# Optimization experiments

Measured on AMD Instinct MI355X. Metric: run time of the kernel, lower is better.

## Reference

```python
import jax, jax.numpy as jnp
import numpy as np

N_NODES = 30000
IN_DIM = 8
HIDDEN = 64
HEADS1 = 8
OUT_DIM = 8
NEG_SLOPE = 0.2


def _glorot(key, shape):
    fan_in, fan_out = shape[0], shape[-1]
    lim = jnp.sqrt(6.0 / (fan_in + fan_out))
    return jax.random.uniform(key, shape, jnp.float32, -lim, lim)


def setup_inputs() -> dict:
    key = jax.random.key(0)
    ks = jax.random.split(key, 12)
    x = jax.random.normal(ks[0], (N_NODES, IN_DIM), jnp.float32)
    edge_index = jax.random.randint(ks[1], (2, 300000), 0, N_NODES, jnp.int32)
    # layer 1: in=8, out=HIDDEN per head, 8 heads, concat
    W1l = _glorot(ks[2], (IN_DIM, HEADS1 * HIDDEN))
    W1r = _glorot(ks[3], (IN_DIM, HEADS1 * HIDDEN))
    a1 = _glorot(ks[4], (HEADS1, HIDDEN))
    b1 = jnp.zeros((HEADS1 * HIDDEN,), jnp.float32)
    # layer 2: in=HEADS1*HIDDEN, out=OUT_DIM, 1 head
    W2l = _glorot(ks[5], (HEADS1 * HIDDEN, OUT_DIM))
    W2r = _glorot(ks[6], (HEADS1 * HIDDEN, OUT_DIM))
    a2 = _glorot(ks[7], (1, OUT_DIM))
    b2 = jnp.zeros((OUT_DIM,), jnp.float32)
    return {"x": x, "edge_index": edge_index, "W1l": W1l, "W1r": W1r,
            "a1": a1, "b1": b1, "W2l": W2l, "W2r": W2r, "a2": a2, "b2": b2}


def gatv2_layer(x, src, dst, Wl, Wr, att, bias, heads, out_ch):
    n = x.shape[0]
    xl = (x @ Wl).reshape(n, heads, out_ch)   # messages (source side)
    xr = (x @ Wr).reshape(n, heads, out_ch)   # target side
    h = jax.nn.leaky_relu(xl[src] + xr[dst], NEG_SLOPE)   # [E,H,C]
    e = jnp.einsum('ehc,hc->eh', h, att)                  # [E,H]
    # segment softmax over incoming edges per destination node
    m = jax.ops.segment_max(e, dst, num_segments=n)
    p = jnp.exp(e - m[dst])
    denom = jax.ops.segment_sum(p, dst, num_segments=n)
    alpha = p / denom[dst]                                # [E,H]
    out = jax.ops.segment_sum(alpha[..., None] * xl[src], dst, num_segments=n)
    return out.reshape(n, heads * out_ch) + bias


def reference(x, edge_index, W1l, W1r, a1, b1, W2l, W2r, a2, b2):
    n = x.shape[0]
    loops = jnp.arange(n, dtype=edge_index.dtype)
    src = jnp.concatenate([edge_index[0], loops])  # add_self_loops=True (PyG default)
    dst = jnp.concatenate([edge_index[1], loops])
    h = gatv2_layer(x, src, dst, W1l, W1r, a1, b1, HEADS1, HIDDEN)
    h = jax.nn.relu(h)
    out = gatv2_layer(h, src, dst, W2l, W2r, a2, b2, 1, OUT_DIM)
    return out
```

## Files before the change

### kernel.cpp

```cpp
#include <hip/hip_runtime.h>
#include <math.h>

#define N_NODES   30000
#define N_EDGE    300000
#define N_EDGE_T  330000
#define HEADS     8
#define HIDDEN    64
#define IN_DIM    8
#define OUT_DIM   8
#define NEG_SLOPE 0.2f
#define MAX_STAGE 64

typedef float v2f __attribute__((ext_vector_type(2)));


__global__ __launch_bounds__(256) void count_kernel(const int* __restrict__ ei,
                                                    int* __restrict__ count) {
    int e = blockIdx.x * 256 + threadIdx.x;
    if (e >= N_EDGE_T) return;
    int d = (e < N_EDGE) ? ei[N_EDGE + e] : (e - N_EDGE);
    atomicAdd(&count[d], 1);
}

__global__ __launch_bounds__(1024) void scan_kernel(const int* __restrict__ count,
                                                    int* __restrict__ row_start,
                                                    int* __restrict__ cursor) {
    __shared__ int wsum[16];
    const int tid  = threadIdx.x;
    const int wave = tid >> 6;
    const int lane = tid & 63;
    const int4* c4 = (const int4*)count;
    const int N4 = N_NODES / 4;
    int run = 0;
    for (int r = 0; r < 4; ++r) {
        const int g  = r * 1024 + tid;
        const int i0 = 2 * g;
        const int i1 = 2 * g + 1;
        int4 v0 = make_int4(0,0,0,0), v1 = make_int4(0,0,0,0);
        if (i0 < N4) v0 = c4[i0];
        if (i1 < N4) v1 = c4[i1];
        int s = v0.x + v0.y + v0.z + v0.w + v1.x + v1.y + v1.z + v1.w;
        int sc = s;
        #pragma unroll
        for (int off = 1; off < 64; off <<= 1) {
            int t = __shfl_up(sc, off, 64);
            if (lane >= off) sc += t;
        }
        if (lane == 63) wsum[wave] = sc;
        __syncthreads();
        if (tid < 16) {
            int w = wsum[tid];
            #pragma unroll
            for (int off = 1; off < 16; off <<= 1) {
                int t = __shfl_up(w, off, 64);
                if (tid >= off) w += t;
            }
            wsum[tid] = w;
        }
        __syncthreads();
        const int woff = (wave > 0) ? wsum[wave - 1] : 0;
        int e0 = run + woff + (sc - s);
        int4 ex0, ex1;
        ex0.x = e0;           ex0.y = ex0.x + v0.x;
        ex0.z = ex0.y + v0.y; ex0.w = ex0.z + v0.z;
        int e4 = ex0.w + v0.w;
        ex1.x = e4;           ex1.y = ex1.x + v1.x;
        ex1.z = ex1.y + v1.y; ex1.w = ex1.z + v1.z;
        if (i0 < N4) { ((int4*)row_start)[i0] = ex0; ((int4*)cursor)[i0] = ex0; }
        if (i1 < N4) { ((int4*)row_start)[i1] = ex1; ((int4*)cursor)[i1] = ex1; }
        const int tot = wsum[15];
        __syncthreads();
        run += tot;
    }
    if (tid == 0) row_start[N_NODES] = run;
}

__global__ __launch_bounds__(256) void scatter_kernel(const int* __restrict__ ei,
                                                      int* __restrict__ cursor,
                                                      int* __restrict__ edge_src) {
    int e = blockIdx.x * 256 + threadIdx.x;
    if (e >= N_EDGE_T) return;
    int s, d;
    if (e < N_EDGE) { s = ei[e]; d = ei[N_EDGE + e]; }
    else            { s = d = e - N_EDGE; }
    int pos = atomicAdd(&cursor[d], 1);
    edge_src[pos] = s;
}


__device__ __forceinline__ void l1_batch(const float xf[4][IN_DIM],
                                         const v2f wl[IN_DIM][2],
                                         const v2f av0, const v2f av1,
                                         const v2f xr0, const v2f xr1,
                                         int nvalid,
                                         float& denom, v2f& acc0, v2f& acc1)
{
    v2f xl[4][2];
    #pragma unroll
    for (int e = 0; e < 4; ++e) { xl[e][0] = v2f{0.f, 0.f}; xl[e][1] = v2f{0.f, 0.f}; }
    #pragma unroll
    for (int k = 0; k < IN_DIM; ++k) {
        #pragma unroll
        for (int e = 0; e < 4; ++e) {
            v2f xs = {xf[e][k], xf[e][k]};
            xl[e][0] = __builtin_elementwise_fma(xs, wl[k][0], xl[e][0]);
            xl[e][1] = __builtin_elementwise_fma(xs, wl[k][1], xl[e][1]);
        }
    }
    float eh[4];
    #pragma unroll
    for (int e = 0; e < 4; ++e) {
        v2f v0 = xl[e][0] + xr0;
        v2f v1 = xl[e][1] + xr1;
        v2f t0 = __builtin_elementwise_max(v0, v0 * NEG_SLOPE);
        v2f t1 = __builtin_elementwise_max(v1, v1 * NEG_SLOPE);
        v2f s2 = __builtin_elementwise_fma(av1, t1, av0 * t0);
        eh[e] = s2.x + s2.y;
    }
    #pragma unroll
    for (int off = 1; off < 16; off <<= 1) {
        #pragma unroll
        for (int e = 0; e < 4; ++e) eh[e] += __shfl_xor(eh[e], off, 64);
    }
    float p[4];
    #pragma unroll
    for (int e = 0; e < 4; ++e) p[e] = (e < nvalid) ? __expf(eh[e]) : 0.f;
    denom += (p[0] + p[1]) + (p[2] + p[3]);
    #pragma unroll
    for (int e = 0; e < 4; ++e) {
        v2f ps = {p[e], p[e]};
        acc0 = __builtin_elementwise_fma(ps, xl[e][0], acc0);
        acc1 = __builtin_elementwise_fma(ps, xl[e][1], acc1);
    }
}

__global__ __launch_bounds__(256, 4) void layer1_kernel(
    const float* __restrict__ x,
    const float* __restrict__ W1l, const float* __restrict__ W1r,
    const float* __restrict__ a1,  const float* __restrict__ b1,
    const float* __restrict__ W2l, const float* __restrict__ W2r,
    const int* __restrict__ row_start, const int* __restrict__ edge_src,
    float* __restrict__ xl2, float* __restrict__ xr2)
{
    __shared__ float lds_x[2][MAX_STAGE][IN_DIM];
    __shared__ float lds_red[2][HEADS][16];

    const int tid  = threadIdx.x;
    const int node = tid >> 7;
    const int t128 = tid & 127;
    const int head = t128 >> 4;
    const int c4   = t128 & 15;
    const int d    = blockIdx.x * 2 + node;
    const int colb = head * HIDDEN + c4 * 4;

    const int rs = row_start[d];
    const int re = row_start[d + 1];
    const int rowlen = re - rs;

    {
        const int slot = t128 >> 1, half = t128 & 1;
        int idx = rs + slot; if (idx > N_EDGE_T - 1) idx = N_EDGE_T - 1;
        const int s = edge_src[idx];
        const float4 v = *(const float4*)(x + s * IN_DIM + half * 4);
        *(float4*)&lds_x[node][slot][half * 4] = v;
    }

    v2f wl[IN_DIM][2], av0, av1;
    #pragma unroll
    for (int k = 0; k < IN_DIM; ++k) {
        const float4 l4 = *(const float4*)&W1l[k * 512 + colb];
        wl[k][0] = v2f{l4.x, l4.y};
        wl[k][1] = v2f{l4.z, l4.w};
    }
    { const float4 a4 = *(const float4*)&a1[colb];
      av0 = v2f{a4.x, a4.y}; av1 = v2f{a4.z, a4.w}; }

    v2f xr0 = v2f{0.f, 0.f}, xr1 = v2f{0.f, 0.f};
    #pragma unroll
    for (int k = 0; k < IN_DIM; ++k) {
        const float xv = x[d * IN_DIM + k];
        const float4 r4 = *(const float4*)&W1r[k * 512 + colb];
        v2f xs = {xv, xv};
        xr0 = __builtin_elementwise_fma(xs, v2f{r4.x, r4.y}, xr0);
        xr1 = __builtin_elementwise_fma(xs, v2f{r4.z, r4.w}, xr1);
    }

    __syncthreads();

    float denom = 0.f;
    v2f acc0 = v2f{0.f, 0.f}, acc1 = v2f{0.f, 0.f};

    const int n_stage = rowlen < MAX_STAGE ? rowlen : MAX_STAGE;
    for (int base = 0; base < n_stage; base += 4) {
        float xf[4][IN_DIM];
        #pragma unroll
        for (int e = 0; e < 4; ++e) {
            int slot = base + e; if (slot > MAX_STAGE - 1) slot = MAX_STAGE - 1;
            const float4 u0 = *(const float4*)&lds_x[node][slot][0];
            const float4 u1 = *(const float4*)&lds_x[node][slot][4];
            xf[e][0] = u0.x; xf[e][1] = u0.y; xf[e][2] = u0.z; xf[e][3] = u0.w;
            xf[e][4] = u1.x; xf[e][5] = u1.y; xf[e][6] = u1.z; xf[e][7] = u1.w;
        }
        l1_batch(xf, wl, av0, av1, xr0, xr1, rowlen - base, denom, acc0, acc1);
    }
    for (int base = MAX_STAGE; base < rowlen; base += 4) {
        float xf[4][IN_DIM];
        #pragma unroll
        for (int e = 0; e < 4; ++e) {
            int idx = rs + base + e; if (idx > re - 1) idx = re - 1;
            const int s = edge_src[idx];
            const float4 u0 = *(const float4*)(x + s * IN_DIM);
            const float4 u1 = *(const float4*)(x + s * IN_DIM + 4);
            xf[e][0] = u0.x; xf[e][1] = u0.y; xf[e][2] = u0.z; xf[e][3] = u0.w;
            xf[e][4] = u1.x; xf[e][5] = u1.y; xf[e][6] = u1.z; xf[e][7] = u1.w;
        }
        l1_batch(xf, wl, av0, av1, xr0, xr1, rowlen - base, denom, acc0, acc1);
    }

    const float inv = 1.f / denom;
    const float4 b4 = *(const float4*)&b1[colb];
    float hv[4];
    hv[0] = fmaxf(acc0.x * inv + b4.x, 0.f);
    hv[1] = fmaxf(acc0.y * inv + b4.y, 0.f);
    hv[2] = fmaxf(acc1.x * inv + b4.z, 0.f);
    hv[3] = fmaxf(acc1.y * inv + b4.w, 0.f);

    float w[16];
    #pragma unroll
    for (int j = 0; j < 16; ++j) w[j] = 0.f;
    #pragma unroll
    for (int i = 0; i < 4; ++i) {
        const float4 l0 = *(const float4*)&W2l[(colb + i) * OUT_DIM];
        const float4 l1 = *(const float4*)&W2l[(colb + i) * OUT_DIM + 4];
        const float4 r0 = *(const float4*)&W2r[(colb + i) * OUT_DIM];
        const float4 r1 = *(const float4*)&W2r[(colb + i) * OUT_DIM + 4];
        w[0]  = fmaf(hv[i], l0.x, w[0]);  w[1]  = fmaf(hv[i], l0.y, w[1]);
        w[2]  = fmaf(hv[i], l0.z, w[2]);  w[3]  = fmaf(hv[i], l0.w, w[3]);
        w[4]  = fmaf(hv[i], l1.x, w[4]);  w[5]  = fmaf(hv[i], l1.y, w[5]);
        w[6]  = fmaf(hv[i], l1.z, w[6]);  w[7]  = fmaf(hv[i], l1.w, w[7]);
        w[8]  = fmaf(hv[i], r0.x, w[8]);  w[9]  = fmaf(hv[i], r0.y, w[9]);
        w[10] = fmaf(hv[i], r0.z, w[10]); w[11] = fmaf(hv[i], r0.w, w[11]);
        w[12] = fmaf(hv[i], r1.x, w[12]); w[13] = fmaf(hv[i], r1.y, w[13]);
        w[14] = fmaf(hv[i], r1.z, w[14]); w[15] = fmaf(hv[i], r1.w, w[15]);
    }
    {
        const bool up = (c4 & 8) != 0;
        #pragma unroll
        for (int i = 0; i < 8; ++i) {
            float send = up ? w[i] : w[i + 8];
            float recv = __shfl_xor(send, 8, 64);
            w[i] = (up ? w[i + 8] : w[i]) + recv;
        }
    }
    {
        const bool up = (c4 & 4) != 0;
        #pragma unroll
        for (int i = 0; i < 4; ++i) {
            float send = up ? w[i] : w[i + 4];
            float recv = __shfl_xor(send, 4, 64);
            w[i] = (up ? w[i + 4] : w[i]) + recv;
        }
    }
    {
        const bool up = (c4 & 2) != 0;
        #pragma unroll
        for (int i = 0; i < 2; ++i) {
            float send = up ? w[i] : w[i + 2];
            float recv = __shfl_xor(send, 2, 64);
            w[i] = (up ? w[i + 2] : w[i]) + recv;
        }
    }
    {
        const bool up = (c4 & 1) != 0;
        float send = up ? w[0] : w[1];
        float recv = __shfl_xor(send, 1, 64);
        w[0] = (up ? w[1] : w[0]) + recv;
    }
    lds_red[node][head][c4] = w[0];
    __syncthreads();
    if (t128 < 16) {
        float s = 0.f;
        #pragma unroll
        for (int h = 0; h < HEADS; ++h) s += lds_red[node][h][t128];
        const int side = t128 >> 3, j = t128 & 7;
        if (side == 0) xl2[d * OUT_DIM + j] = s;
        else           xr2[d * OUT_DIM + j] = s;
    }
}


__global__ __launch_bounds__(256) void layer2_kernel(
    const float* __restrict__ xl2, const float* __restrict__ xr2,
    const float* __restrict__ a2,  const float* __restrict__ b2,
    const int* __restrict__ row_start, const int* __restrict__ edge_src,
    float* __restrict__ out)
{
    const int wave = threadIdx.x >> 6;
    const int lane = threadIdx.x & 63;
    const int d = blockIdx.x * 4 + wave;
    if (d >= N_NODES) return;
    const int sub = lane >> 3;
    const int c   = lane & 7;

    const float a_c  = a2[c];
    const float xr_d = xr2[d * OUT_DIM + c];

    const int rs = row_start[d];
    const int re = row_start[d + 1];

    float denom = 0.f, acc = 0.f;

    for (int base = rs; base < re; base += 8) {
        int e = base + sub;
        bool valid = (e < re);
        int s = valid ? edge_src[e] : 0;
        float xls = xl2[s * OUT_DIM + c];
        float v = xls + xr_d;
        float t = fmaxf(v, NEG_SLOPE * v);
        float eh = a_c * t;
        eh += __shfl_xor(eh, 1, 64);
        eh += __shfl_xor(eh, 2, 64);
        eh += __shfl_xor(eh, 4, 64);
        float p = valid ? __expf(eh) : 0.f;
        denom += p;
        acc = fmaf(p, xls, acc);
    }

    denom += __shfl_xor(denom, 8,  64);  acc += __shfl_xor(acc, 8,  64);
    denom += __shfl_xor(denom, 16, 64);  acc += __shfl_xor(acc, 16, 64);
    denom += __shfl_xor(denom, 32, 64);  acc += __shfl_xor(acc, 32, 64);

    if (sub == 0) out[d * OUT_DIM + c] = acc / denom + b2[c];
}


extern "C" void kernel_launch(void* const* d_in, const int* in_sizes, int n_in,
                              void* d_out, int out_size, void* d_ws, size_t ws_size,
                              hipStream_t stream) {
    const float* x   = (const float*)d_in[0];
    const int*   ei  = (const int*)  d_in[1];
    const float* W1l = (const float*)d_in[2];
    const float* W1r = (const float*)d_in[3];
    const float* a1  = (const float*)d_in[4];
    const float* b1  = (const float*)d_in[5];
    const float* W2l = (const float*)d_in[6];
    const float* W2r = (const float*)d_in[7];
    const float* a2  = (const float*)d_in[8];
    const float* b2  = (const float*)d_in[9];
    float* out = (float*)d_out;

    char* ws = (char*)d_ws;
    size_t off = 0;
    auto carve = [&](size_t bytes) { char* p = ws + off; off += (bytes + 255) & ~size_t(255); return p; };
    int*   count     = (int*)  carve(N_NODES * sizeof(int));
    int*   row_start = (int*)  carve((N_NODES + 1) * sizeof(int));
    int*   cursor    = (int*)  carve(N_NODES * sizeof(int));
    int*   edge_src  = (int*)  carve((N_EDGE_T + 8) * sizeof(int));
    float* xl2       = (float*)carve(N_NODES * OUT_DIM * sizeof(float));
    float* xr2       = (float*)carve(N_NODES * OUT_DIM * sizeof(float));

    hipMemsetAsync(count, 0, N_NODES * sizeof(int), stream);
    count_kernel  <<<(N_EDGE_T + 255) / 256, 256, 0, stream>>>(ei, count);
    scan_kernel   <<<1, 1024, 0, stream>>>(count, row_start, cursor);
    scatter_kernel<<<(N_EDGE_T + 255) / 256, 256, 0, stream>>>(ei, cursor, edge_src);
    layer1_kernel <<<N_NODES / 2, 256, 0, stream>>>(x, W1l, W1r, a1, b1, W2l, W2r,
                                                    row_start, edge_src, xl2, xr2);
    layer2_kernel <<<(N_NODES + 3) / 4, 256, 0, stream>>>(xl2, xr2, a2, b2,
                                                          row_start, edge_src, out);
}
```

Baseline: 277.5 us.

## Pre-gather source features in CSR order and use persistent wave-per-half-node layer kernels

The scatter kernel now copies each edge's source feature row into a CSR-ordered buffer, so layer 1 streams contiguous features instead of doing an indirect gather through LDS staging. Layer 1 becomes a grid-stride persistent kernel where each wave handles four heads of one node. Per-head partial layer-2 projections are combined with atomicAdd into zeroed xl2/xr2, which removes the LDS reduction and block syncs. Layer 2 also becomes grid-stride. The cost is an extra ~10 MB write and read of gathered features, plus atomics and float summation order that is no longer deterministic.

```diff
diff --git a/kernel.cpp b/kernel.cpp
--- a/kernel.cpp
+++ b/kernel.cpp
@@ -9,7 +9,6 @@
 #define IN_DIM    8
 #define OUT_DIM   8
 #define NEG_SLOPE 0.2f
-#define MAX_STAGE 64
 
 typedef float v2f __attribute__((ext_vector_type(2)));
 
@@ -77,7 +76,9 @@
 
 __global__ __launch_bounds__(256) void scatter_kernel(const int* __restrict__ ei,
                                                       int* __restrict__ cursor,
-                                                      int* __restrict__ edge_src) {
+                                                      int* __restrict__ edge_src,
+                                                      const float* __restrict__ x,
+                                                      float* __restrict__ xg) {
     int e = blockIdx.x * 256 + threadIdx.x;
     if (e >= N_EDGE_T) return;
     int s, d;
@@ -85,206 +86,172 @@
     else            { s = d = e - N_EDGE; }
     int pos = atomicAdd(&cursor[d], 1);
     edge_src[pos] = s;
-}
-
-
-__device__ __forceinline__ void l1_batch(const float xf[4][IN_DIM],
-                                         const v2f wl[IN_DIM][2],
-                                         const v2f av0, const v2f av1,
-                                         const v2f xr0, const v2f xr1,
-                                         int nvalid,
-                                         float& denom, v2f& acc0, v2f& acc1)
-{
-    v2f xl[4][2];
-    #pragma unroll
-    for (int e = 0; e < 4; ++e) { xl[e][0] = v2f{0.f, 0.f}; xl[e][1] = v2f{0.f, 0.f}; }
-    #pragma unroll
-    for (int k = 0; k < IN_DIM; ++k) {
-        #pragma unroll
-        for (int e = 0; e < 4; ++e) {
-            v2f xs = {xf[e][k], xf[e][k]};
-            xl[e][0] = __builtin_elementwise_fma(xs, wl[k][0], xl[e][0]);
-            xl[e][1] = __builtin_elementwise_fma(xs, wl[k][1], xl[e][1]);
-        }
-    }
-    float eh[4];
-    #pragma unroll
-    for (int e = 0; e < 4; ++e) {
-        v2f v0 = xl[e][0] + xr0;
-        v2f v1 = xl[e][1] + xr1;
-        v2f t0 = __builtin_elementwise_max(v0, v0 * NEG_SLOPE);
-        v2f t1 = __builtin_elementwise_max(v1, v1 * NEG_SLOPE);
-        v2f s2 = __builtin_elementwise_fma(av1, t1, av0 * t0);
-        eh[e] = s2.x + s2.y;
-    }
-    #pragma unroll
-    for (int off = 1; off < 16; off <<= 1) {
-        #pragma unroll
-        for (int e = 0; e < 4; ++e) eh[e] += __shfl_xor(eh[e], off, 64);
-    }
-    float p[4];
-    #pragma unroll
-    for (int e = 0; e < 4; ++e) p[e] = (e < nvalid) ? __expf(eh[e]) : 0.f;
-    denom += (p[0] + p[1]) + (p[2] + p[3]);
-    #pragma unroll
-    for (int e = 0; e < 4; ++e) {
-        v2f ps = {p[e], p[e]};
-        acc0 = __builtin_elementwise_fma(ps, xl[e][0], acc0);
-        acc1 = __builtin_elementwise_fma(ps, xl[e][1], acc1);
-    }
-}
+    const float4* xs = (const float4*)(x + s * IN_DIM);
+    float4 a = xs[0], b = xs[1];
+    float4* dst = (float4*)(xg + pos * IN_DIM);
+    dst[0] = a; dst[1] = b;
+}
+
 
 __global__ __launch_bounds__(256, 4) void layer1_kernel(
     const float* __restrict__ x,
     const float* __restrict__ W1l, const float* __restrict__ W1r,
     const float* __restrict__ a1,  const float* __restrict__ b1,
     const float* __restrict__ W2l, const float* __restrict__ W2r,
-    const int* __restrict__ row_start, const int* __restrict__ edge_src,
+    const int* __restrict__ row_start, const float* __restrict__ xg,
     float* __restrict__ xl2, float* __restrict__ xr2)
 {
-    __shared__ float lds_x[2][MAX_STAGE][IN_DIM];
-    __shared__ float lds_red[2][HEADS][16];
-
-    const int tid  = threadIdx.x;
-    const int node = tid >> 7;
-    const int t128 = tid & 127;
-    const int head = t128 >> 4;
-    const int c4   = t128 & 15;
-    const int d    = blockIdx.x * 2 + node;
-    const int colb = head * HIDDEN + c4 * 4;
-
-    const int rs = row_start[d];
-    const int re = row_start[d + 1];
-    const int rowlen = re - rs;
-
-    {
-        const int slot = t128 >> 1, half = t128 & 1;
-        int idx = rs + slot; if (idx > N_EDGE_T - 1) idx = N_EDGE_T - 1;
-        const int s = edge_src[idx];
-        const float4 v = *(const float4*)(x + s * IN_DIM + half * 4);
-        *(float4*)&lds_x[node][slot][half * 4] = v;
-    }
-
-    v2f wl[IN_DIM][2], av0, av1;
+    const int lane  = threadIdx.x & 63;
+    const int gwave = (blockIdx.x * 256 + threadIdx.x) >> 6;
+    const int nwave = (gridDim.x * 256) >> 6;
+    const int half  = gwave & 1;
+    const int grp   = lane >> 4;
+    const int c4    = lane & 15;
+    const int head  = half * 4 + grp;
+    const int colb  = head * HIDDEN + c4 * 4;
+
+    v2f wl[IN_DIM][2];
     #pragma unroll
     for (int k = 0; k < IN_DIM; ++k) {
         const float4 l4 = *(const float4*)&W1l[k * 512 + colb];
         wl[k][0] = v2f{l4.x, l4.y};
         wl[k][1] = v2f{l4.z, l4.w};
     }
+    v2f av0, av1;
     { const float4 a4 = *(const float4*)&a1[colb];
       av0 = v2f{a4.x, a4.y}; av1 = v2f{a4.z, a4.w}; }
-
-    v2f xr0 = v2f{0.f, 0.f}, xr1 = v2f{0.f, 0.f};
-    #pragma unroll
-    for (int k = 0; k < IN_DIM; ++k) {
-        const float xv = x[d * IN_DIM + k];
-        const float4 r4 = *(const float4*)&W1r[k * 512 + colb];
-        v2f xs = {xv, xv};
-        xr0 = __builtin_elementwise_fma(xs, v2f{r4.x, r4.y}, xr0);
-        xr1 = __builtin_elementwise_fma(xs, v2f{r4.z, r4.w}, xr1);
-    }
-
-    __syncthreads();
-
-    float denom = 0.f;
-    v2f acc0 = v2f{0.f, 0.f}, acc1 = v2f{0.f, 0.f};
-
-    const int n_stage = rowlen < MAX_STAGE ? rowlen : MAX_STAGE;
-    for (int base = 0; base < n_stage; base += 4) {
-        float xf[4][IN_DIM];
+    const float4 b4 = *(const float4*)&b1[colb];
+
+    const float4* g = (const float4*)xg;
+
+    for (int d = gwave >> 1; d < N_NODES; d += nwave >> 1) {
+        const int rs = __builtin_amdgcn_readfirstlane(row_start[d]);
+        const int re = __builtin_amdgcn_readfirstlane(row_start[d + 1]);
+
+        v2f xr0 = v2f{0.f, 0.f}, xr1 = v2f{0.f, 0.f};
         #pragma unroll
-        for (int e = 0; e < 4; ++e) {
-            int slot = base + e; if (slot > MAX_STAGE - 1) slot = MAX_STAGE - 1;
-            const float4 u0 = *(const float4*)&lds_x[node][slot][0];
-            const float4 u1 = *(const float4*)&lds_x[node][slot][4];
-            xf[e][0] = u0.x; xf[e][1] = u0.y; xf[e][2] = u0.z; xf[e][3] = u0.w;
-            xf[e][4] = u1.x; xf[e][5] = u1.y; xf[e][6] = u1.z; xf[e][7] = u1.w;
-        }
-        l1_batch(xf, wl, av0, av1, xr0, xr1, rowlen - base, denom, acc0, acc1);
-    }
-    for (int base = MAX_STAGE; base < rowlen; base += 4) {
-        float xf[4][IN_DIM];
+        for (int k = 0; k < IN_DIM; ++k) {
+            const float xv = x[d * IN_DIM + k];
+            const float4 r4 = *(const float4*)&W1r[k * 512 + colb];
+            v2f xs = {xv, xv};
+            xr0 = __builtin_elementwise_fma(xs, v2f{r4.x, r4.y}, xr0);
+            xr1 = __builtin_elementwise_fma(xs, v2f{r4.z, r4.w}, xr1);
+        }
+
+        float denom = 0.f;
+        v2f acc0 = v2f{0.f, 0.f}, acc1 = v2f{0.f, 0.f};
+
+        for (int base = rs; base < re; base += 4) {
+            float xf[4][IN_DIM];
+            #pragma unroll
+            for (int e = 0; e < 4; ++e) {
+                const float4 u0 = g[(base + e) * 2];
+                const float4 u1 = g[(base + e) * 2 + 1];
+                xf[e][0] = u0.x; xf[e][1] = u0.y; xf[e][2] = u0.z; xf[e][3] = u0.w;
+                xf[e][4] = u1.x; xf[e][5] = u1.y; xf[e][6] = u1.z; xf[e][7] = u1.w;
+            }
+
+            v2f xl[4][2];
+            #pragma unroll
+            for (int e = 0; e < 4; ++e) { xl[e][0] = v2f{0.f, 0.f}; xl[e][1] = v2f{0.f, 0.f}; }
+            #pragma unroll
+            for (int k = 0; k < IN_DIM; ++k) {
+                #pragma unroll
+                for (int e = 0; e < 4; ++e) {
+                    v2f xs = {xf[e][k], xf[e][k]};
+                    xl[e][0] = __builtin_elementwise_fma(xs, wl[k][0], xl[e][0]);
+                    xl[e][1] = __builtin_elementwise_fma(xs, wl[k][1], xl[e][1]);
+                }
+            }
+
+            float eh[4];
+            #pragma unroll
+            for (int e = 0; e < 4; ++e) {
+                v2f v0 = xl[e][0] + xr0;
+                v2f v1 = xl[e][1] + xr1;
+                v2f t0 = __builtin_elementwise_max(v0, v0 * NEG_SLOPE);
+                v2f t1 = __builtin_elementwise_max(v1, v1 * NEG_SLOPE);
+                v2f s2 = __builtin_elementwise_fma(av1, t1, av0 * t0);
+                eh[e] = s2.x + s2.y;
+            }
+            #pragma unroll
+            for (int off = 1; off < 16; off <<= 1) {
+                #pragma unroll
+                for (int e = 0; e < 4; ++e) eh[e] += __shfl_xor(eh[e], off, 64);
+            }
+
+            float p[4];
+            #pragma unroll
+            for (int e = 0; e < 4; ++e)
+                p[e] = (base + e < re) ? __expf(eh[e]) : 0.f;
+
+            denom += (p[0] + p[1]) + (p[2] + p[3]);
+            #pragma unroll
+            for (int e = 0; e < 4; ++e) {
+                v2f ps = {p[e], p[e]};
+                acc0 = __builtin_elementwise_fma(ps, xl[e][0], acc0);
+                acc1 = __builtin_elementwise_fma(ps, xl[e][1], acc1);
+            }
+        }
+
+        const float inv = 1.f / denom;
+        float hv[4];
+        hv[0] = fmaxf(acc0.x * inv + b4.x, 0.f);
+        hv[1] = fmaxf(acc0.y * inv + b4.y, 0.f);
+        hv[2] = fmaxf(acc1.x * inv + b4.z, 0.f);
+        hv[3] = fmaxf(acc1.y * inv + b4.w, 0.f);
+
+        float w[16];
         #pragma unroll
-        for (int e = 0; e < 4; ++e) {
-            int idx = rs + base + e; if (idx > re - 1) idx = re - 1;
-            const int s = edge_src[idx];
-            const float4 u0 = *(const float4*)(x + s * IN_DIM);
-            const float4 u1 = *(const float4*)(x + s * IN_DIM + 4);
-            xf[e][0] = u0.x; xf[e][1] = u0.y; xf[e][2] = u0.z; xf[e][3] = u0.w;
-            xf[e][4] = u1.x; xf[e][5] = u1.y; xf[e][6] = u1.z; xf[e][7] = u1.w;
-        }
-        l1_batch(xf, wl, av0, av1, xr0, xr1, rowlen - base, denom, acc0, acc1);
-    }
-
-    const float inv = 1.f / denom;
-    const float4 b4 = *(const float4*)&b1[colb];
-    float hv[4];
-    hv[0] = fmaxf(acc0.x * inv + b4.x, 0.f);
-    hv[1] = fmaxf(acc0.y * inv + b4.y, 0.f);
-    hv[2] = fmaxf(acc1.x * inv + b4.z, 0.f);
-    hv[3] = fmaxf(acc1.y * inv + b4.w, 0.f);
-
-    float w[16];
-    #pragma unroll
-    for (int j = 0; j < 16; ++j) w[j] = 0.f;
-    #pragma unroll
-    for (int i = 0; i < 4; ++i) {
-        const float4 l0 = *(const float4*)&W2l[(colb + i) * OUT_DIM];
-        const float4 l1 = *(const float4*)&W2l[(colb + i) * OUT_DIM + 4];
-        const float4 r0 = *(const float4*)&W2r[(colb + i) * OUT_DIM];
-        const float4 r1 = *(const float4*)&W2r[(colb + i) * OUT_DIM + 4];
-        w[0]  = fmaf(hv[i], l0.x, w[0]);  w[1]  = fmaf(hv[i], l0.y, w[1]);
-        w[2]  = fmaf(hv[i], l0.z, w[2]);  w[3]  = fmaf(hv[i], l0.w, w[3]);
-        w[4]  = fmaf(hv[i], l1.x, w[4]);  w[5]  = fmaf(hv[i], l1.y, w[5]);
-        w[6]  = fmaf(hv[i], l1.z, w[6]);  w[7]  = fmaf(hv[i], l1.w, w[7]);
-        w[8]  = fmaf(hv[i], r0.x, w[8]);  w[9]  = fmaf(hv[i], r0.y, w[9]);
-        w[10] = fmaf(hv[i], r0.z, w[10]); w[11] = fmaf(hv[i], r0.w, w[11]);
-        w[12] = fmaf(hv[i], r1.x, w[12]); w[13] = fmaf(hv[i], r1.y, w[13]);
-        w[14] = fmaf(hv[i], r1.z, w[14]); w[15] = fmaf(hv[i], r1.w, w[15]);
-    }
-    {
-        const bool up = (c4 & 8) != 0;
-        #pragma unroll
-        for (int i = 0; i < 8; ++i) {
-            float send = up ? w[i] : w[i + 8];
-            float recv = __shfl_xor(send, 8, 64);
-            w[i] = (up ? w[i + 8] : w[i]) + recv;
-        }
-    }
-    {
-        const bool up = (c4 & 4) != 0;
+        for (int j = 0; j < 16; ++j) w[j] = 0.f;
         #pragma unroll
         for (int i = 0; i < 4; ++i) {
-            float send = up ? w[i] : w[i + 4];
-            float recv = __shfl_xor(send, 4, 64);
-            w[i] = (up ? w[i + 4] : w[i]) + recv;
-        }
-    }
-    {
-        const bool up = (c4 & 2) != 0;
-        #pragma unroll
-        for (int i = 0; i < 2; ++i) {
-            float send = up ? w[i] : w[i + 2];
-            float recv = __shfl_xor(send, 2, 64);
-            w[i] = (up ? w[i + 2] : w[i]) + recv;
-        }
-    }
-    {
-        const bool up = (c4 & 1) != 0;
-        float send = up ? w[0] : w[1];
-        float recv = __shfl_xor(send, 1, 64);
-        w[0] = (up ? w[1] : w[0]) + recv;
-    }
-    lds_red[node][head][c4] = w[0];
-    __syncthreads();
-    if (t128 < 16) {
-        float s = 0.f;
-        #pragma unroll
-        for (int h = 0; h < HEADS; ++h) s += lds_red[node][h][t128];
-        const int side = t128 >> 3, j = t128 & 7;
-        if (side == 0) xl2[d * OUT_DIM + j] = s;
-        else           xr2[d * OUT_DIM + j] = s;
+            const float4 l0 = *(const float4*)&W2l[(colb + i) * OUT_DIM];
+            const float4 l1 = *(const float4*)&W2l[(colb + i) * OUT_DIM + 4];
+            const float4 r0 = *(const float4*)&W2r[(colb + i) * OUT_DIM];
+            const float4 r1 = *(const float4*)&W2r[(colb + i) * OUT_DIM + 4];
+            w[0]  = fmaf(hv[i], l0.x, w[0]);  w[1]  = fmaf(hv[i], l0.y, w[1]);
+            w[2]  = fmaf(hv[i], l0.z, w[2]);  w[3]  = fmaf(hv[i], l0.w, w[3]);
+            w[4]  = fmaf(hv[i], l1.x, w[4]);  w[5]  = fmaf(hv[i], l1.y, w[5]);
+            w[6]  = fmaf(hv[i], l1.z, w[6]);  w[7]  = fmaf(hv[i], l1.w, w[7]);
+            w[8]  = fmaf(hv[i], r0.x, w[8]);  w[9]  = fmaf(hv[i], r0.y, w[9]);
+            w[10] = fmaf(hv[i], r0.z, w[10]); w[11] = fmaf(hv[i], r0.w, w[11]);
+            w[12] = fmaf(hv[i], r1.x, w[12]); w[13] = fmaf(hv[i], r1.y, w[13]);
+            w[14] = fmaf(hv[i], r1.z, w[14]); w[15] = fmaf(hv[i], r1.w, w[15]);
+        }
+        {   const bool up = (c4 & 8) != 0;
+            #pragma unroll
+            for (int i = 0; i < 8; ++i) {
+                float send = up ? w[i] : w[i + 8];
+                float recv = __shfl_xor(send, 8, 64);
+                w[i] = (up ? w[i + 8] : w[i]) + recv;
+            } }
+        {   const bool up = (c4 & 4) != 0;
+            #pragma unroll
+            for (int i = 0; i < 4; ++i) {
+                float send = up ? w[i] : w[i + 4];
+                float recv = __shfl_xor(send, 4, 64);
+                w[i] = (up ? w[i + 4] : w[i]) + recv;
+            } }
+        {   const bool up = (c4 & 2) != 0;
+            #pragma unroll
+            for (int i = 0; i < 2; ++i) {
+                float send = up ? w[i] : w[i + 2];
+                float recv = __shfl_xor(send, 2, 64);
+                w[i] = (up ? w[i + 2] : w[i]) + recv;
+            } }
+        {   const bool up = (c4 & 1) != 0;
+            float send = up ? w[0] : w[1];
+            float recv = __shfl_xor(send, 1, 64);
+            w[0] = (up ? w[1] : w[0]) + recv;
+        }
+        w[0] += __shfl_xor(w[0], 16, 64);
+        w[0] += __shfl_xor(w[0], 32, 64);
+        if (lane < 16) {
+            float* dst = (lane < 8) ? &xl2[d * OUT_DIM + lane]
+                                    : &xr2[d * OUT_DIM + (lane - 8)];
+            atomicAdd(dst, w[0]);
+        }
     }
 }
 
@@ -295,42 +262,41 @@
     const int* __restrict__ row_start, const int* __restrict__ edge_src,
     float* __restrict__ out)
 {
-    const int wave = threadIdx.x >> 6;
-    const int lane = threadIdx.x & 63;
-    const int d = blockIdx.x * 4 + wave;
-    if (d >= N_NODES) return;
+    const int lane  = threadIdx.x & 63;
+    const int gwave = (blockIdx.x * 256 + threadIdx.x) >> 6;
+    const int nwave = (gridDim.x * 256) >> 6;
     const int sub = lane >> 3;
     const int c   = lane & 7;
 
-    const float a_c  = a2[c];
-    const float xr_d = xr2[d * OUT_DIM + c];
-
-    const int rs = row_start[d];
-    const int re = row_start[d + 1];
-
-    float denom = 0.f, acc = 0.f;
-
-    for (int base = rs; base < re; base += 8) {
-        int e = base + sub;
-        bool valid = (e < re);
-        int s = valid ? edge_src[e] : 0;
-        float xls = xl2[s * OUT_DIM + c];
-        float v = xls + xr_d;
-        float t = fmaxf(v, NEG_SLOPE * v);
-        float eh = a_c * t;
-        eh += __shfl_xor(eh, 1, 64);
-        eh += __shfl_xor(eh, 2, 64);
-        eh += __shfl_xor(eh, 4, 64);
-        float p = valid ? __expf(eh) : 0.f;
-        denom += p;
-        acc = fmaf(p, xls, acc);
+    const float a_c = a2[c];
+    const float b_c = b2[c];
+
+    for (int d = gwave; d < N_NODES; d += nwave) {
+        const float xr_d = xr2[d * OUT_DIM + c];
+        const int rs = row_start[d];
+        const int re = row_start[d + 1];
+
+        float denom = 0.f, acc = 0.f;
+        for (int base = rs; base < re; base += 8) {
+            int e = base + sub;
+            bool valid = (e < re);
+            int s = valid ? edge_src[e] : 0;
+            float xls = xl2[s * OUT_DIM + c];
+            float v = xls + xr_d;
+            float t = fmaxf(v, NEG_SLOPE * v);
+            float eh = a_c * t;
+            eh += __shfl_xor(eh, 1, 64);
+            eh += __shfl_xor(eh, 2, 64);
+            eh += __shfl_xor(eh, 4, 64);
+            float p = valid ? __expf(eh) : 0.f;
+            denom += p;
+            acc = fmaf(p, xls, acc);
+        }
+        denom += __shfl_xor(denom, 8,  64);  acc += __shfl_xor(acc, 8,  64);
+        denom += __shfl_xor(denom, 16, 64);  acc += __shfl_xor(acc, 16, 64);
+        denom += __shfl_xor(denom, 32, 64);  acc += __shfl_xor(acc, 32, 64);
+        if (sub == 0) out[d * OUT_DIM + c] = acc / denom + b_c;
     }
-
-    denom += __shfl_xor(denom, 8,  64);  acc += __shfl_xor(acc, 8,  64);
-    denom += __shfl_xor(denom, 16, 64);  acc += __shfl_xor(acc, 16, 64);
-    denom += __shfl_xor(denom, 32, 64);  acc += __shfl_xor(acc, 32, 64);
-
-    if (sub == 0) out[d * OUT_DIM + c] = acc / denom + b2[c];
 }
 
 
@@ -353,18 +319,20 @@
     size_t off = 0;
     auto carve = [&](size_t bytes) { char* p = ws + off; off += (bytes + 255) & ~size_t(255); return p; };
     int*   count     = (int*)  carve(N_NODES * sizeof(int));
+    float* xl2       = (float*)carve(N_NODES * OUT_DIM * sizeof(float));
+    float* xr2       = (float*)carve(N_NODES * OUT_DIM * sizeof(float));
+    size_t zero_span = off;
     int*   row_start = (int*)  carve((N_NODES + 1) * sizeof(int));
     int*   cursor    = (int*)  carve(N_NODES * sizeof(int));
     int*   edge_src  = (int*)  carve((N_EDGE_T + 8) * sizeof(int));
-    float* xl2       = (float*)carve(N_NODES * OUT_DIM * sizeof(float));
-    float* xr2       = (float*)carve(N_NODES * OUT_DIM * sizeof(float));
-
-    hipMemsetAsync(count, 0, N_NODES * sizeof(int), stream);
+    float* xg        = (float*)carve((N_EDGE_T + 8) * IN_DIM * sizeof(float));
+
+    hipMemsetAsync(count, 0, zero_span, stream);
     count_kernel  <<<(N_EDGE_T + 255) / 256, 256, 0, stream>>>(ei, count);
     scan_kernel   <<<1, 1024, 0, stream>>>(count, row_start, cursor);
-    scatter_kernel<<<(N_EDGE_T + 255) / 256, 256, 0, stream>>>(ei, cursor, edge_src);
-    layer1_kernel <<<N_NODES / 2, 256, 0, stream>>>(x, W1l, W1r, a1, b1, W2l, W2r,
-                                                    row_start, edge_src, xl2, xr2);
-    layer2_kernel <<<(N_NODES + 3) / 4, 256, 0, stream>>>(xl2, xr2, a2, b2,
-                                                          row_start, edge_src, out);
-}
+    scatter_kernel<<<(N_EDGE_T + 255) / 256, 256, 0, stream>>>(ei, cursor, edge_src, x, xg);
+    layer1_kernel <<<1024, 256, 0, stream>>>(x, W1l, W1r, a1, b1, W2l, W2r,
+                                             row_start, xg, xl2, xr2);
+    layer2_kernel <<<512, 256, 0, stream>>>(xl2, xr2, a2, b2,
+                                            row_start, edge_src, out);
+}
```

Result: slower. 295.8 us (+6.6%).
